# Kernel optimization log

Measured on AMD Instinct MI355X. Metric: run time of the kernel, lower is better.

Reference implementation:

```python
import jax, jax.numpy as jnp
from jax import lax
import numpy as np

BETA = 0.9   # snn.Leaky(beta=0.9)
THR = 1.0    # snntorch default threshold, reset_mechanism='subtract'

@jax.custom_vjp
def spike(x):
    return (x > 0.0).astype(x.dtype)

def _spike_fwd(x):
    return spike(x), x

def _spike_bwd(x, g):
    # snntorch surrogate.atan (alpha=2): dS/dx = 1 / (1 + (pi*x)^2)
    return (g / (1.0 + (jnp.pi * x) ** 2),)

spike.defvjp(_spike_fwd, _spike_bwd)

def lif(inp, mem):
    # snntorch Leaky: reset based on PREVIOUS mem, detached; subtract mechanism
    reset = lax.stop_gradient(spike(mem - THR))
    mem = BETA * mem + inp - reset * THR
    return spike(mem - THR), mem

def conv1d(x, w, b):
    # x: (B, Cin, L), w: (Cout, Cin, K), VALID padding
    y = lax.conv_general_dilated(x, w, window_strides=(1,), padding='VALID',
                                 dimension_numbers=('NCH', 'OIH', 'NCH'))
    return y + b[None, :, None]

def setup_inputs() -> dict:
    key = jax.random.key(0)
    ks = jax.random.split(key, 11)
    B, L, T, num_c = 1024, 30, 100, 10
    def init(k, shape, fan_in):
        bound = 1.0 / np.sqrt(fan_in)
        return jax.random.uniform(k, shape, jnp.float32, -bound, bound)
    return {
        'x':   jax.random.normal(ks[0], (B, 1, L, T), jnp.float32),
        'w1':  init(ks[1], (16, 1, 7), 1 * 7),   'b1': init(ks[2], (16,), 7),
        'w2':  init(ks[3], (32, 16, 5), 16 * 5), 'b2': init(ks[4], (32,), 80),
        'w3':  init(ks[5], (64, 32, 3), 32 * 3), 'b3': init(ks[6], (64,), 96),
        'fw1': init(ks[7], (256, 64 * 18), 64 * 18), 'fb1': init(ks[8], (256,), 64 * 18),
        'fw2': init(ks[9], (num_c, 256), 256),       'fb2': init(ks[10], (num_c,), 256),
    }

def reference(x, w1, b1, w2, b2, w3, b3, fw1, fb1, fw2, fb2):
    B = x.shape[0]
    num_c = fw2.shape[0]
    xt_seq = jnp.transpose(x, (3, 0, 1, 2))  # (T, B, 1, 30)
    mems = (jnp.zeros((B, 16, 24), x.dtype),  # after conv1 (k=7): 30->24
            jnp.zeros((B, 32, 20), x.dtype),  # after conv2 (k=5): 24->20
            jnp.zeros((B, 64, 18), x.dtype),  # after conv3 (k=3): 20->18
            jnp.zeros((B, 256), x.dtype),
            jnp.zeros((B, num_c), x.dtype))
    def step(mems, xt):
        m1, m2, m3, m4, m5 = mems
        h = conv1d(xt, w1, b1); s, m1 = lif(h, m1)
        h = conv1d(s, w2, b2);  s, m2 = lif(h, m2)
        h = conv1d(s, w3, b3);  s, m3 = lif(h, m3)
        h = s.reshape(B, -1) @ fw1.T + fb1; s, m4 = lif(h, m4)
        h = s @ fw2.T + fb2;               s, m5 = lif(h, m5)
        return (m1, m2, m3, m4, m5), s
    _, spk_rec = lax.scan(step, mems, xt_seq)
    return spk_rec  # (T, B, num_c) -- matches torch.stack(spk_rec)
```

## Files before the change

### kernel.cpp

```cpp
#include <hip/hip_runtime.h>
#include <stdint.h>

#define BETA 0.9f

__global__ void transpose_fw1(const float* __restrict__ A, float* __restrict__ At) {
    __shared__ float tile[32][33];
    const int i0 = blockIdx.x * 32;
    const int j0 = blockIdx.y * 32;
    const int tx = threadIdx.x, ty = threadIdx.y;
    for (int r = ty; r < 32; r += 8)
        tile[r][tx] = A[(j0 + r) * 1152 + i0 + tx];
    __syncthreads();
    for (int r = ty; r < 32; r += 8)
        At[(i0 + r) * 256 + j0 + tx] = tile[tx][r];
}

__global__ __launch_bounds__(768)
__attribute__((amdgpu_waves_per_eu(6)))
void snn_main(
    const float* __restrict__ x,
    const float* __restrict__ w1, const float* __restrict__ b1,
    const float* __restrict__ w2, const float* __restrict__ b2,
    const float* __restrict__ w3, const float* __restrict__ b3,
    const float* __restrict__ fw1T,
    const float* __restrict__ fb1,
    const float* __restrict__ fw2, const float* __restrict__ fb2,
    float* __restrict__ out)
{
    const int b    = blockIdx.x;
    const int tid  = threadIdx.x;
    const int e    = (tid >= 384) ? 1 : 0;
    const int tl   = tid - 384 * e;
    const int lane = tid & 63;
    const int ew   = tl >> 6;

    __shared__ float w2L[16 * 5 * 32];
    __shared__ float w3L[32 * 3 * 64];
    __shared__ float pacc[2][6][256];
    __shared__ float s1e[2][16 * 24 + 8];
    __shared__ float s4[2][256];
    __shared__ unsigned long long masks[2][18];
    __shared__ unsigned int rm1[2][2][16];
    __shared__ unsigned int cm2[2][2][20];

    const int c1 = tl & 15;
    const int l1 = tl >> 4;
    const int c2 = tl & 31;
    const int g2 = tl >> 5;
    const int l02 = (g2 < 8) ? 2 * g2 : 16 + (g2 - 8);
    const int nl2 = (g2 < 8) ? 2 : 1;
    const int c3 = lane;
    const int l03 = ew * 3;
    const unsigned wmask2 = (ew < 4)  ? (0xFFu << (4 * ew)) :
                            (ew == 4) ? 0x3F0000u :
                                        0xFC0000u;

    for (int i = tid; i < 16 * 5 * 32; i += 768) {
        const int cc = i & 31, r = i >> 5;
        w2L[i] = w2[cc * 80 + r];
    }
    for (int i = tid; i < 32 * 3 * 64; i += 768) {
        const int cc = i & 63, r = i >> 6;
        w3L[i] = w3[cc * 96 + r];
    }
    if (tl < 16) { rm1[e][0][tl] = 0u; rm1[e][1][tl] = 0u; }
    if (tl < 20) { cm2[e][0][tl] = 0u; cm2[e][1][tl] = 0u; }
    if (tl < 8)  s1e[e][384 + tl] = 0.0f;

    float w1r[7];
#pragma unroll
    for (int k = 0; k < 7; ++k) w1r[k] = w1[c1 * 7 + k];
    const float b1r = b1[c1];
    const float b2r = b2[c2];
    const float b3r = b3[c3];
    const float fb1r = (tl < 256) ? fb1[tl] : 0.0f;
    const int jf = tl >> 4, chf = tl & 15;
    const float fb2r = (tl < 160 && chf == 0) ? fb2[jf] : 0.0f;

    float m1 = 0.f;
    float m2[2] = {0.f, 0.f};
    float m3[3] = {0.f, 0.f, 0.f};
    float m4 = 0.f, m5 = 0.f;

    const float* xb = x + (2 * b + e) * 3000;
    const int out_b = (2 * b + e) * 10;
    const float4* fw1Tv = reinterpret_cast<const float4*>(fw1T);

    float xr[7];
#pragma unroll
    for (int k = 0; k < 7; ++k) xr[k] = xb[(l1 + k) * 100];

    __syncthreads();

    for (int t = 0; t < 100; ++t) {
        const int pb = t & 1, pn = pb ^ 1;

        {
            float h = b1r;
#pragma unroll
            for (int k = 0; k < 7; ++k) h += xr[k] * w1r[k];
            float rs = (m1 > 1.0f) ? 1.0f : 0.0f;
            m1 = BETA * m1 + h - rs;
            float sa = (m1 > 1.0f) ? 1.0f : 0.0f;
            s1e[e][c1 * 24 + l1] = sa;
            if (sa != 0.0f) atomicOr(&rm1[e][pb][c1], 1u << l1);
            const int tt = (t < 99) ? t + 1 : 99;
#pragma unroll
            for (int k = 0; k < 7; ++k) xr[k] = xb[(l1 + k) * 100 + tt];
        }
        __syncthreads();

        {
            if (tl < 16) rm1[e][pn][tl] = 0u;
            if (tl < 20) cm2[e][pn][tl] = 0u;
            float h[2] = {b2r, b2r};
#pragma unroll
            for (int ci = 0; ci < 16; ++ci) {
                const unsigned rmv =
                    __builtin_amdgcn_readfirstlane(rm1[e][pb][ci]);
                if ((rmv & wmask2) == 0u) continue;
                float win[6];
#pragma unroll
                for (int r = 0; r < 6; ++r) win[r] = s1e[e][ci * 24 + l02 + r];
                float wk[5];
#pragma unroll
                for (int k = 0; k < 5; ++k) wk[k] = w2L[(ci * 5 + k) * 32 + c2];
#pragma unroll
                for (int li = 0; li < 2; ++li)
                    if (li < nl2)
#pragma unroll
                        for (int k = 0; k < 5; ++k) h[li] += win[li + k] * wk[k];
            }
#pragma unroll
            for (int li = 0; li < 2; ++li)
                if (li < nl2) {
                    float rs = (m2[li] > 1.0f) ? 1.0f : 0.0f;
                    m2[li] = BETA * m2[li] + h[li] - rs;
                    if (m2[li] > 1.0f) atomicOr(&cm2[e][pb][l02 + li], 1u << c2);
                }
        }
        __syncthreads();

        {
            float h[3] = {b3r, b3r, b3r};
#pragma unroll
            for (int wl = 0; wl < 5; ++wl) {
                unsigned cm = __builtin_amdgcn_readfirstlane(cm2[e][pb][l03 + wl]);
                while (cm) {
                    const int ci = (int)__builtin_ctz(cm); cm &= cm - 1;
                    const float* wp = &w3L[ci * 192 + c3];
#pragma unroll
                    for (int k = 0; k < 3; ++k) {
                        const int li = wl - k;
                        if (li >= 0 && li < 3)
                            h[li] += wp[k * 64];
                    }
                }
            }
#pragma unroll
            for (int li = 0; li < 3; ++li) {
                float rs = (m3[li] > 1.0f) ? 1.0f : 0.0f;
                m3[li] = BETA * m3[li] + h[li] - rs;
                float s = (m3[li] > 1.0f) ? 1.0f : 0.0f;
                unsigned long long mk = __ballot(s != 0.0f);
                if (lane == 0) masks[e][l03 + li] = mk;
            }
        }
        __syncthreads();

        {
            float4 acc4; acc4.x = acc4.y = acc4.z = acc4.w = 0.0f;
#pragma unroll 1
            for (int l = ew; l < 18; l += 6) {
                const unsigned* mp = (const unsigned*)&masks[e][l];
                const unsigned mlo = __builtin_amdgcn_readfirstlane(mp[0]);
                const unsigned mhi = __builtin_amdgcn_readfirstlane(mp[1]);
                unsigned long long mk = ((unsigned long long)mhi << 32) | mlo;
                while (mk) {
                    float4 f0, f1, f2, f3;
                    f0.x=f0.y=f0.z=f0.w=0.f; f1=f0; f2=f0; f3=f0;
                    int c;
                    c = (int)__builtin_ctzll(mk); mk &= mk - 1;
                    f0 = fw1Tv[(c * 18 + l) * 64 + lane];
                    if (mk) { c = (int)__builtin_ctzll(mk); mk &= mk - 1;
                              f1 = fw1Tv[(c * 18 + l) * 64 + lane]; }
                    if (mk) { c = (int)__builtin_ctzll(mk); mk &= mk - 1;
                              f2 = fw1Tv[(c * 18 + l) * 64 + lane]; }
                    if (mk) { c = (int)__builtin_ctzll(mk); mk &= mk - 1;
                              f3 = fw1Tv[(c * 18 + l) * 64 + lane]; }
                    acc4.x += f0.x; acc4.y += f0.y; acc4.z += f0.z; acc4.w += f0.w;
                    acc4.x += f1.x; acc4.y += f1.y; acc4.z += f1.z; acc4.w += f1.w;
                    acc4.x += f2.x; acc4.y += f2.y; acc4.z += f2.z; acc4.w += f2.w;
                    acc4.x += f3.x; acc4.y += f3.y; acc4.z += f3.z; acc4.w += f3.w;
                }
            }
            ((float4*)&pacc[e][ew][0])[lane] = acc4;
        }
        __syncthreads();

        if (tl < 256) {
            float acc = fb1r;
#pragma unroll
            for (int w = 0; w < 6; ++w) acc += pacc[e][w][tl];
            float rs = (m4 > 1.0f) ? 1.0f : 0.0f;
            m4 = BETA * m4 + acc - rs;
            s4[e][tl] = (m4 > 1.0f) ? 1.0f : 0.0f;
        }
        __syncthreads();

        if (tl < 160) {
            const float* wrow = fw2 + jf * 256;
            float p = 0.f;
#pragma unroll
            for (int i = 0; i < 16; ++i)
                p += s4[e][i * 16 + chf] * wrow[i * 16 + chf];
            p += __shfl_xor(p, 8, 16);
            p += __shfl_xor(p, 4, 16);
            p += __shfl_xor(p, 2, 16);
            p += __shfl_xor(p, 1, 16);
            if (chf == 0) {
                float h = fb2r + p;
                float rs = (m5 > 1.0f) ? 1.0f : 0.0f;
                m5 = BETA * m5 + h - rs;
                out[t * 10240 + out_b + jf] = (m5 > 1.0f) ? 1.0f : 0.0f;
            }
        }
    }
}

extern "C" void kernel_launch(void* const* d_in, const int* in_sizes, int n_in,
                              void* d_out, int out_size, void* d_ws, size_t ws_size,
                              hipStream_t stream) {
    const float* x   = (const float*)d_in[0];
    const float* w1  = (const float*)d_in[1];
    const float* b1  = (const float*)d_in[2];
    const float* w2  = (const float*)d_in[3];
    const float* b2  = (const float*)d_in[4];
    const float* w3  = (const float*)d_in[5];
    const float* b3  = (const float*)d_in[6];
    const float* fw1 = (const float*)d_in[7];
    const float* fb1 = (const float*)d_in[8];
    const float* fw2 = (const float*)d_in[9];
    const float* fb2 = (const float*)d_in[10];
    float* out  = (float*)d_out;
    float* fw1T = (float*)d_ws;

    dim3 tb(32, 8);
    dim3 tg(1152 / 32, 256 / 32);
    transpose_fw1<<<tg, tb, 0, stream>>>(fw1, fw1T);
    snn_main<<<512, 768, 0, stream>>>(x, w1, b1, w2, b2, w3, b3,
                                      fw1T, fb1, fw2, fb2, out);
}
```

Before: 647.0 us.

## Software-pipeline conv1 into previous step's FC phase and vectorize conv2 window loads

Moves the conv1+LIF stage for timestep t+1 to after the conv3 barrier of step t, so it runs in the same barrier interval as the FC1 phase and removes one __syncthreads per timestep. The x prefetch moves into the conv2 phase. Conv2 is remapped so each of 10 thread groups handles two consecutive output positions, with float2 shared loads and explicit FMAs, replacing the uneven 2/1 split. The risks are s1e being rewritten while conv2 might still read it, which the ordering relies on barriers to prevent, and misaligned float2 loads if the offsets are odd.

```diff
diff --git a/kernel.cpp b/kernel.cpp
--- a/kernel.cpp
+++ b/kernel.cpp
@@ -47,13 +47,11 @@
     const int l1 = tl >> 4;
     const int c2 = tl & 31;
     const int g2 = tl >> 5;
-    const int l02 = (g2 < 8) ? 2 * g2 : 16 + (g2 - 8);
-    const int nl2 = (g2 < 8) ? 2 : 1;
+    const int l02 = 2 * g2;
+    const bool c2on = (g2 < 10);
+    const unsigned wmask2 = c2on ? (0x3Fu << l02) : 0u;
     const int c3 = lane;
     const int l03 = ew * 3;
-    const unsigned wmask2 = (ew < 4)  ? (0xFFu << (4 * ew)) :
-                            (ew == 4) ? 0x3F0000u :
-                                        0xFC0000u;
 
     for (int i = tid; i < 16 * 5 * 32; i += 768) {
         const int cc = i & 31, r = i >> 5;
@@ -92,52 +90,55 @@
 
     __syncthreads();
 
+    {
+        float h = b1r;
+#pragma unroll
+        for (int k = 0; k < 7; ++k) h += xr[k] * w1r[k];
+        float rs = (m1 > 1.0f) ? 1.0f : 0.0f;
+        m1 = BETA * m1 + h - rs;
+        float sa = (m1 > 1.0f) ? 1.0f : 0.0f;
+        s1e[e][c1 * 24 + l1] = sa;
+        if (sa != 0.0f) atomicOr(&rm1[e][0][c1], 1u << l1);
+    }
+    __syncthreads();
+
     for (int t = 0; t < 100; ++t) {
         const int pb = t & 1, pn = pb ^ 1;
-
-        {
-            float h = b1r;
-#pragma unroll
-            for (int k = 0; k < 7; ++k) h += xr[k] * w1r[k];
-            float rs = (m1 > 1.0f) ? 1.0f : 0.0f;
-            m1 = BETA * m1 + h - rs;
-            float sa = (m1 > 1.0f) ? 1.0f : 0.0f;
-            s1e[e][c1 * 24 + l1] = sa;
-            if (sa != 0.0f) atomicOr(&rm1[e][pb][c1], 1u << l1);
-            const int tt = (t < 99) ? t + 1 : 99;
-#pragma unroll
-            for (int k = 0; k < 7; ++k) xr[k] = xb[(l1 + k) * 100 + tt];
-        }
-        __syncthreads();
 
         {
             if (tl < 16) rm1[e][pn][tl] = 0u;
             if (tl < 20) cm2[e][pn][tl] = 0u;
+            if (t < 99) {
+#pragma unroll
+                for (int k = 0; k < 7; ++k) xr[k] = xb[(l1 + k) * 100 + t + 1];
+            }
             float h[2] = {b2r, b2r};
 #pragma unroll
             for (int ci = 0; ci < 16; ++ci) {
                 const unsigned rmv =
                     __builtin_amdgcn_readfirstlane(rm1[e][pb][ci]);
                 if ((rmv & wmask2) == 0u) continue;
-                float win[6];
-#pragma unroll
-                for (int r = 0; r < 6; ++r) win[r] = s1e[e][ci * 24 + l02 + r];
+                const float2* wp2 =
+                    (const float2*)&s1e[e][ci * 24 + l02];
+                const float2 wa = wp2[0], wb = wp2[1], wc = wp2[2];
                 float wk[5];
 #pragma unroll
                 for (int k = 0; k < 5; ++k) wk[k] = w2L[(ci * 5 + k) * 32 + c2];
-#pragma unroll
-                for (int li = 0; li < 2; ++li)
-                    if (li < nl2)
-#pragma unroll
-                        for (int k = 0; k < 5; ++k) h[li] += win[li + k] * wk[k];
-            }
-#pragma unroll
-            for (int li = 0; li < 2; ++li)
-                if (li < nl2) {
+                h[0] += wa.x * wk[0]; h[0] += wa.y * wk[1];
+                h[0] += wb.x * wk[2]; h[0] += wb.y * wk[3];
+                h[0] += wc.x * wk[4];
+                h[1] += wa.y * wk[0]; h[1] += wb.x * wk[1];
+                h[1] += wb.y * wk[2]; h[1] += wc.x * wk[3];
+                h[1] += wc.y * wk[4];
+            }
+            if (c2on) {
+#pragma unroll
+                for (int li = 0; li < 2; ++li) {
                     float rs = (m2[li] > 1.0f) ? 1.0f : 0.0f;
                     m2[li] = BETA * m2[li] + h[li] - rs;
                     if (m2[li] > 1.0f) atomicOr(&cm2[e][pb][l02 + li], 1u << c2);
                 }
+            }
         }
         __syncthreads();
 
@@ -167,6 +168,17 @@
             }
         }
         __syncthreads();
+
+        if (t < 99) {
+            float h = b1r;
+#pragma unroll
+            for (int k = 0; k < 7; ++k) h += xr[k] * w1r[k];
+            float rs = (m1 > 1.0f) ? 1.0f : 0.0f;
+            m1 = BETA * m1 + h - rs;
+            float sa = (m1 > 1.0f) ? 1.0f : 0.0f;
+            s1e[e][c1 * 24 + l1] = sa;
+            if (sa != 0.0f) atomicOr(&rm1[e][pn][c1], 1u << l1);
+        }
 
         {
             float4 acc4; acc4.x = acc4.y = acc4.z = acc4.w = 0.0f;
```

Measured after the change: 622.0 us. 1.04x faster.
